# Kernel tuning notes

Hardware: AMD Instinct MI355X
Metric: run time of the kernel (lower is better)

Reference implementation:

```python
import jax, jax.numpy as jnp
import numpy as np

EPS = 1e-4
MAX_LAPLACE_VAR = 1000.0
MAX_DENSITY = 10000.0
BINS = 256

_LAP_KERNEL = jnp.array([[0., 1., 0.], [1., -4., 1.], [0., 1., 0.]], dtype=jnp.float32)[None, None]  # OIHW [1,1,3,3]


def setup_inputs() -> dict:
    key = jax.random.key(0)
    k1, k2 = jax.random.split(key)
    rgb_img = jax.random.uniform(k1, (32, 3, 512, 512), dtype=jnp.float32)
    depth_img = jax.random.normal(k2, (32, 1, 512, 512), dtype=jnp.float32)
    return {"rgb_img": rgb_img, "depth_img": depth_img}


def _rgb_confidence(rgb_img):
    B, C, H, W = rgb_img.shape
    gray = 0.299 * rgb_img[:, 0] + 0.587 * rgb_img[:, 1] + 0.114 * rgb_img[:, 2]  # [B,H,W]
    gray = gray[:, None]  # [B,1,H,W]
    lap = jax.lax.conv_general_dilated(
        gray, _LAP_KERNEL, window_strides=(1, 1), padding=[(1, 1), (1, 1)],
        dimension_numbers=("NCHW", "OIHW", "NCHW"))
    # torch.var default is unbiased (ddof=1)
    laplace_var = jnp.var(lap, axis=(1, 2, 3), ddof=1)

    # integer-valued pixels 0..255 land exactly in histc bins 0..255 (bins=256, min=0, max=255)
    vals = jnp.clip(gray * 255.0, 0.0, 255.0).astype(jnp.int32)  # [B,1,H,W]
    vals = vals.reshape(B, -1)  # [B, H*W]
    bidx = jnp.broadcast_to(jnp.arange(B)[:, None], vals.shape)
    hist = jnp.zeros((B, BINS), jnp.float32).at[bidx, vals].add(1.0)
    p = hist / jnp.sum(hist, axis=1, keepdims=True)
    entropy = -jnp.sum(p * jnp.log2(p + EPS), axis=1)

    clarity_score = laplace_var / (MAX_LAPLACE_VAR + EPS)
    uniformity_score = 1.0 / (entropy + EPS)
    return (0.5 * (clarity_score + uniformity_score))[:, None]  # [B,1]


def _depth_confidence(depth_img):
    C = depth_img.shape[1]
    depth_map = depth_img[:, 2] if C == 3 else depth_img[:, 0]  # [B,H,W]
    mask = (depth_map > 0).astype(jnp.float32)
    density = jnp.mean(mask, axis=(1, 2))

    # vectorized masked std (unbiased, ddof=1), matching torch.std over valid pixels
    n = jnp.sum(mask, axis=(1, 2))  # [B]
    mean = jnp.sum(depth_map * mask, axis=(1, 2)) / jnp.maximum(n, 1.0)
    sq = jnp.sum(mask * (depth_map - mean[:, None, None]) ** 2, axis=(1, 2))
    var = sq / jnp.maximum(n - 1.0, 1.0)
    std = jnp.sqrt(jnp.maximum(var, 0.0))
    noise_level = jnp.where(n > 0, std, 1.0)

    density_score = density / (MAX_DENSITY + EPS)
    noise_score = 1.0 / (noise_level + EPS)
    return (0.5 * (density_score + noise_score))[:, None]  # [B,1]


def reference(rgb_img, depth_img):
    rgb_conf = _rgb_confidence(rgb_img)
    depth_conf = _depth_confidence(depth_img)
    denom = rgb_conf + depth_conf + EPS
    w_r = rgb_conf / denom
    w_d = depth_conf / denom
    return (w_r, w_d)
```

## Files before the change

kernel.cpp:

```cpp
#include <hip/hip_runtime.h>

#define IMG_H 512
#define IMG_W 512
#define HW (IMG_H * IMG_W)
#define NB 32
#define STRIPS 16
#define RPW 8

#define ACC_DOUBLES 160
#define WS_BYTES (ACC_DOUBLES * 8 + NB * 256 * 4)

struct Row6 { float4 a0, a1, b0, b1, c0, c1; };

__device__ inline Row6 load_row(const float* __restrict__ rp, int r, int c0) {
    Row6 x;
    if ((unsigned)r < IMG_H) {
        const size_t o = (size_t)r * IMG_W + c0;
        x.a0 = *(const float4*)(rp + o);
        x.a1 = *(const float4*)(rp + o + 4);
        x.b0 = *(const float4*)(rp + HW + o);
        x.b1 = *(const float4*)(rp + HW + o + 4);
        x.c0 = *(const float4*)(rp + 2 * HW + o);
        x.c1 = *(const float4*)(rp + 2 * HW + o + 4);
    } else {
        const float4 z = {0.f, 0.f, 0.f, 0.f};
        x.a0 = x.a1 = x.b0 = x.b1 = x.c0 = x.c1 = z;
    }
    return x;
}

__device__ inline void to_gray(const Row6& x, float g[8]) {
    g[0] = 0.299f * x.a0.x + 0.587f * x.b0.x + 0.114f * x.c0.x;
    g[1] = 0.299f * x.a0.y + 0.587f * x.b0.y + 0.114f * x.c0.y;
    g[2] = 0.299f * x.a0.z + 0.587f * x.b0.z + 0.114f * x.c0.z;
    g[3] = 0.299f * x.a0.w + 0.587f * x.b0.w + 0.114f * x.c0.w;
    g[4] = 0.299f * x.a1.x + 0.587f * x.b1.x + 0.114f * x.c1.x;
    g[5] = 0.299f * x.a1.y + 0.587f * x.b1.y + 0.114f * x.c1.y;
    g[6] = 0.299f * x.a1.z + 0.587f * x.b1.z + 0.114f * x.c1.z;
    g[7] = 0.299f * x.a1.w + 0.587f * x.b1.w + 0.114f * x.c1.w;
}

__global__ __launch_bounds__(256, 2) void fused_kernel(
    const float* __restrict__ rgb, const float* __restrict__ depth,
    double* __restrict__ acc, unsigned int* __restrict__ hist)
{
    __shared__ unsigned int lh[4][256];
    __shared__ double red[4][5];

    const int t = threadIdx.x;
    const int b = blockIdx.y;
    const int s = blockIdx.x;
    const int lane = t & 63;
    const int w = t >> 6;

    #pragma unroll
    for (int i = 0; i < 4; ++i) lh[i][t & 255] = 0u;
    __syncthreads();

    const float* rp = rgb + (size_t)b * 3 * HW;
    const int rb = s * 32 + w * RPW;
    const int c0 = lane * 8;

    const float4* dp = (const float4*)(depth + (size_t)b * HW + (size_t)s * (HW / STRIPS));

    Row6 r0 = load_row(rp, rb - 1, c0);
    Row6 r1 = load_row(rp, rb, c0);
    Row6 buf[3];
    float4 dv[3][2];
    buf[0] = load_row(rp, rb + 1, c0); dv[0][0] = dp[0 * 256 + t]; dv[0][1] = dp[1 * 256 + t];
    buf[1] = load_row(rp, rb + 2, c0); dv[1][0] = dp[2 * 256 + t]; dv[1][1] = dp[3 * 256 + t];
    buf[2] = load_row(rp, rb + 3, c0); dv[2][0] = dp[4 * 256 + t]; dv[2][1] = dp[5 * 256 + t];

    float gp[8], gc[8], gn[8];
    to_gray(r0, gp);
    to_gray(r1, gc);

    float s1 = 0.f, s2 = 0.f;
    float dnf = 0.f, dsf = 0.f, dqf = 0.f;

    #pragma unroll
    for (int r = 0; r < RPW; ++r) {
        const int bi = r % 3;
        to_gray(buf[bi], gn);
        const float4 d0 = dv[bi][0];
        const float4 d1 = dv[bi][1];

        if (r < RPW - 3) {
            buf[bi] = load_row(rp, rb + r + 4, c0);
            dv[bi][0] = dp[(2 * r + 6) * 256 + t];
            dv[bi][1] = dp[(2 * r + 7) * 256 + t];
        }

        float lf = __shfl_up(gc[7], 1, 64);
        if (lane == 0) lf = 0.f;
        float rt = __shfl_down(gc[0], 1, 64);
        if (lane == 63) rt = 0.f;

        #pragma unroll
        for (int j = 0; j < 8; ++j) {
            const float left  = (j == 0) ? lf : gc[j - 1];
            const float right = (j == 7) ? rt : gc[j + 1];
            const float lap = gp[j] + gn[j] + left + right - 4.f * gc[j];
            s1 += lap;
            s2 += lap * lap;
            atomicAdd(&lh[w][(int)fminf(fmaxf(gc[j] * 255.f, 0.f), 255.f)], 1u);
        }

        if (d0.x > 0.f) { dnf += 1.f; dsf += d0.x; dqf += d0.x * d0.x; }
        if (d0.y > 0.f) { dnf += 1.f; dsf += d0.y; dqf += d0.y * d0.y; }
        if (d0.z > 0.f) { dnf += 1.f; dsf += d0.z; dqf += d0.z * d0.z; }
        if (d0.w > 0.f) { dnf += 1.f; dsf += d0.w; dqf += d0.w * d0.w; }
        if (d1.x > 0.f) { dnf += 1.f; dsf += d1.x; dqf += d1.x * d1.x; }
        if (d1.y > 0.f) { dnf += 1.f; dsf += d1.y; dqf += d1.y * d1.y; }
        if (d1.z > 0.f) { dnf += 1.f; dsf += d1.z; dqf += d1.z * d1.z; }
        if (d1.w > 0.f) { dnf += 1.f; dsf += d1.w; dqf += d1.w * d1.w; }

        #pragma unroll
        for (int j = 0; j < 8; ++j) { gp[j] = gc[j]; gc[j] = gn[j]; }
    }

    double z0 = (double)s1, z1 = (double)s2, z2 = (double)dnf, z3 = (double)dsf, z4 = (double)dqf;
    for (int off = 32; off > 0; off >>= 1) {
        z0 += __shfl_down(z0, off, 64);
        z1 += __shfl_down(z1, off, 64);
        z2 += __shfl_down(z2, off, 64);
        z3 += __shfl_down(z3, off, 64);
        z4 += __shfl_down(z4, off, 64);
    }
    if (lane == 0) {
        red[w][0] = z0; red[w][1] = z1; red[w][2] = z2; red[w][3] = z3; red[w][4] = z4;
    }
    __syncthreads();

    const unsigned int hsum = lh[0][t] + lh[1][t] + lh[2][t] + lh[3][t];
    atomicAdd(&hist[b * 256 + t], hsum);
    if (t < 5) {
        const double v = red[0][t] + red[1][t] + red[2][t] + red[3][t];
        atomicAdd(&acc[t * 32 + b], v);
    }
}

__global__ __launch_bounds__(256) void final_kernel(
    const double* __restrict__ acc,
    const unsigned int* __restrict__ hist,
    float* __restrict__ out)
{
    __shared__ float part[256];
    const int t = threadIdx.x;
    const int b = t >> 3;
    const int sl = t & 7;
    float e = 0.f;
    #pragma unroll
    for (int i = 0; i < 32; ++i) {
        const float p = (float)hist[b * 256 + sl * 32 + i] * (1.0f / (float)HW);
        e += p * log2f(p + 1e-4f);
    }
    part[t] = e;
    __syncthreads();

    if (t < NB) {
        float es = 0.f;
        #pragma unroll
        for (int i = 0; i < 8; ++i) es += part[t * 8 + i];
        const double entropy = -(double)es;
        const double N = (double)HW;

        const double ls = acc[t], lq = acc[32 + t];
        const double lvar = (lq - ls * ls / N) / (N - 1.0);
        const double clarity = lvar / (1000.0 + 1e-4);
        const double uniformity = 1.0 / (entropy + 1e-4);
        const double rgb_conf = 0.5 * (clarity + uniformity);

        const double n = acc[64 + t], sdep = acc[96 + t], q = acc[128 + t];
        const double mean = sdep / fmax(n, 1.0);
        const double sq = q - 2.0 * mean * sdep + mean * mean * n;
        const double var = sq / fmax(n - 1.0, 1.0);
        const double stdd = sqrt(fmax(var, 0.0));
        const double noise = (n > 0.0) ? stdd : 1.0;
        const double density = n / N;
        const double depth_conf = 0.5 * (density / (10000.0 + 1e-4) + 1.0 / (noise + 1e-4));

        const double denom = rgb_conf + depth_conf + 1e-4;
        out[t]      = (float)(rgb_conf / denom);
        out[NB + t] = (float)(depth_conf / denom);
    }
}

extern "C" void kernel_launch(void* const* d_in, const int* in_sizes, int n_in,
                              void* d_out, int out_size, void* d_ws, size_t ws_size,
                              hipStream_t stream) {
    const float* rgb   = (const float*)d_in[0];
    const float* depth = (const float*)d_in[1];
    float* out = (float*)d_out;

    double* acc = (double*)d_ws;
    unsigned int* hist = (unsigned int*)((char*)d_ws + ACC_DOUBLES * 8);

    hipMemsetAsync(d_ws, 0, WS_BYTES, stream);

    fused_kernel<<<dim3(STRIPS, NB), 256, 0, stream>>>(rgb, depth, acc, hist);
    final_kernel<<<1, 256, 0, stream>>>(acc, hist, out);
}
```

Measured before the change: 179.2 us.

## Fuse final reduction into main kernel via last-block counter and double strips

Measured after the change: 360.0 us. 2.01x slower.

```diff
diff --git a/kernel.cpp b/kernel.cpp
--- a/kernel.cpp
+++ b/kernel.cpp
@@ -4,11 +4,12 @@
 #define IMG_W 512
 #define HW (IMG_H * IMG_W)
 #define NB 32
-#define STRIPS 16
-#define RPW 8
+#define STRIPS 32
+#define RPW 4
 
 #define ACC_DOUBLES 160
-#define WS_BYTES (ACC_DOUBLES * 8 + NB * 256 * 4)
+#define HIST_U32 (NB * 256)
+#define WS_BYTES (ACC_DOUBLES * 8 + HIST_U32 * 4 + NB * 4)
 
 struct Row6 { float4 a0, a1, b0, b1, c0, c1; };
 
@@ -40,12 +41,23 @@
     g[7] = 0.299f * x.a1.w + 0.587f * x.b1.w + 0.114f * x.c1.w;
 }
 
-__global__ __launch_bounds__(256, 2) void fused_kernel(
+__device__ inline double agent_load_d(const double* p) {
+    unsigned long long v = __hip_atomic_load((const unsigned long long*)p,
+                                             __ATOMIC_RELAXED, __HIP_MEMORY_SCOPE_AGENT);
+    return __longlong_as_double(v);
+}
+__device__ inline unsigned int agent_load_u(const unsigned int* p) {
+    return __hip_atomic_load(p, __ATOMIC_RELAXED, __HIP_MEMORY_SCOPE_AGENT);
+}
+
+__global__ __launch_bounds__(256, 4) void fused_kernel(
     const float* __restrict__ rgb, const float* __restrict__ depth,
-    double* __restrict__ acc, unsigned int* __restrict__ hist)
+    double* __restrict__ acc, unsigned int* __restrict__ hist,
+    unsigned int* __restrict__ cnt, float* __restrict__ out)
 {
     __shared__ unsigned int lh[4][256];
     __shared__ double red[4][5];
+    __shared__ unsigned int lastflag;
 
     const int t = threadIdx.x;
     const int b = blockIdx.y;
@@ -54,11 +66,11 @@
     const int w = t >> 6;
 
     #pragma unroll
-    for (int i = 0; i < 4; ++i) lh[i][t & 255] = 0u;
+    for (int i = 0; i < 4; ++i) lh[i][t] = 0u;
     __syncthreads();
 
     const float* rp = rgb + (size_t)b * 3 * HW;
-    const int rb = s * 32 + w * RPW;
+    const int rb = s * (4 * RPW) + w * RPW;
     const int c0 = lane * 8;
 
     const float4* dp = (const float4*)(depth + (size_t)b * HW + (size_t)s * (HW / STRIPS));
@@ -138,40 +150,37 @@
         const double v = red[0][t] + red[1][t] + red[2][t] + red[3][t];
         atomicAdd(&acc[t * 32 + b], v);
     }
-}
-
-__global__ __launch_bounds__(256) void final_kernel(
-    const double* __restrict__ acc,
-    const unsigned int* __restrict__ hist,
-    float* __restrict__ out)
-{
-    __shared__ float part[256];
-    const int t = threadIdx.x;
-    const int b = t >> 3;
-    const int sl = t & 7;
-    float e = 0.f;
-    #pragma unroll
-    for (int i = 0; i < 32; ++i) {
-        const float p = (float)hist[b * 256 + sl * 32 + i] * (1.0f / (float)HW);
-        e += p * log2f(p + 1e-4f);
-    }
-    part[t] = e;
-    __syncthreads();
-
-    if (t < NB) {
-        float es = 0.f;
-        #pragma unroll
-        for (int i = 0; i < 8; ++i) es += part[t * 8 + i];
-        const double entropy = -(double)es;
+
+    __threadfence();
+    __syncthreads();
+    if (t == 0) {
+        const unsigned int old = atomicAdd(&cnt[b], 1u);
+        lastflag = (old == STRIPS - 1) ? 1u : 0u;
+    }
+    __syncthreads();
+    if (lastflag == 0u) return;
+    __threadfence();
+
+    const unsigned int hv = agent_load_u(&hist[b * 256 + t]);
+    const float p = (float)hv * (1.0f / (float)HW);
+    double term = (double)(p * log2f(p + 1e-4f));
+    for (int off = 32; off > 0; off >>= 1) term += __shfl_down(term, off, 64);
+    if (lane == 0) red[w][0] = term;
+    __syncthreads();
+
+    if (t == 0) {
+        const double entropy = -(red[0][0] + red[1][0] + red[2][0] + red[3][0]);
         const double N = (double)HW;
 
-        const double ls = acc[t], lq = acc[32 + t];
+        const double ls = agent_load_d(&acc[b]), lq = agent_load_d(&acc[32 + b]);
         const double lvar = (lq - ls * ls / N) / (N - 1.0);
         const double clarity = lvar / (1000.0 + 1e-4);
         const double uniformity = 1.0 / (entropy + 1e-4);
         const double rgb_conf = 0.5 * (clarity + uniformity);
 
-        const double n = acc[64 + t], sdep = acc[96 + t], q = acc[128 + t];
+        const double n = agent_load_d(&acc[64 + b]);
+        const double sdep = agent_load_d(&acc[96 + b]);
+        const double q = agent_load_d(&acc[128 + b]);
         const double mean = sdep / fmax(n, 1.0);
         const double sq = q - 2.0 * mean * sdep + mean * mean * n;
         const double var = sq / fmax(n - 1.0, 1.0);
@@ -181,8 +190,8 @@
         const double depth_conf = 0.5 * (density / (10000.0 + 1e-4) + 1.0 / (noise + 1e-4));
 
         const double denom = rgb_conf + depth_conf + 1e-4;
-        out[t]      = (float)(rgb_conf / denom);
-        out[NB + t] = (float)(depth_conf / denom);
+        out[b]      = (float)(rgb_conf / denom);
+        out[NB + b] = (float)(depth_conf / denom);
     }
 }
 
@@ -195,9 +204,9 @@
 
     double* acc = (double*)d_ws;
     unsigned int* hist = (unsigned int*)((char*)d_ws + ACC_DOUBLES * 8);
+    unsigned int* cnt  = (unsigned int*)((char*)d_ws + ACC_DOUBLES * 8 + HIST_U32 * 4);
 
     hipMemsetAsync(d_ws, 0, WS_BYTES, stream);
 
-    fused_kernel<<<dim3(STRIPS, NB), 256, 0, stream>>>(rgb, depth, acc, hist);
-    final_kernel<<<1, 256, 0, stream>>>(acc, hist, out);
-}
+    fused_kernel<<<dim3(STRIPS, NB), 256, 0, stream>>>(rgb, depth, acc, hist, cnt, out);
+}
```
